# Kernel optimization log

Measured on AMD Instinct MI355X. Metric: run time of the kernel, lower is better.

Reference implementation:

```python
import jax, jax.numpy as jnp
import numpy as np

WINDOW_SIZE = 32  # band half-width = 16
EPS = 1e-5       # torch InstanceNorm1d default eps


def instance_norm_t(y):
    # y: (B, T, H); torch InstanceNorm1d (affine=False) normalizes each channel
    # over the temporal axis per sample, biased variance.
    m = jnp.mean(y, axis=1, keepdims=True)
    v = jnp.var(y, axis=1, keepdims=True)
    return (y - m) * jax.lax.rsqrt(v + EPS)


def setup_inputs() -> dict:
    key = jax.random.key(0)
    ks = jax.random.split(key, 7)
    B, T, IN, H = 4, 2048, 256, 256
    x = jax.random.normal(ks[0], (B, T, IN), dtype=jnp.float32)
    s = 0.02
    Wq = jax.random.normal(ks[1], (H, IN), dtype=jnp.float32) * s
    bq = jax.random.normal(ks[2], (H,), dtype=jnp.float32) * s
    Wk = jax.random.normal(ks[3], (H, IN), dtype=jnp.float32) * s
    bk = jax.random.normal(ks[4], (H,), dtype=jnp.float32) * s
    Wv = jax.random.normal(ks[5], (H, IN), dtype=jnp.float32) * s
    bv = jax.random.normal(ks[6], (H,), dtype=jnp.float32) * s
    return {"x": x, "Wq": Wq, "bq": bq, "Wk": Wk, "bk": bk, "Wv": Wv, "bv": bv}


def reference(x, Wq, bq, Wk, bk, Wv, bv):
    B, T, _ = x.shape
    H = Wq.shape[0]
    scale = H ** (-0.5)
    half = WINDOW_SIZE // 2  # 16

    q = instance_norm_t(x @ Wq.T + bq)  # (B, T, H)
    k = instance_norm_t(x @ Wk.T + bk)
    v = instance_norm_t(x @ Wv.T + bv)

    # Banded attention: for each query i only keys j with |i-j| <= half are live.
    offs = jnp.arange(-half, half + 1)                 # (W,) with W = 33
    idx = jnp.arange(T)[:, None] + offs[None, :]       # (T, W)
    valid = (idx >= 0) & (idx < T)                     # (T, W)
    idx_c = jnp.clip(idx, 0, T - 1)

    k_win = k[:, idx_c, :]                             # (B, T, W, H)
    v_win = v[:, idx_c, :]                             # (B, T, W, H)

    scores = jnp.einsum('bth,btwh->btw', q, k_win) * scale
    scores = jnp.where(valid[None], scores, -jnp.inf)
    probs = jax.nn.softmax(scores, axis=-1)            # (B, T, W)
    out = jnp.einsum('btw,btwh->bth', probs, v_win)    # (B, T, H)
    return jnp.mean(out, axis=1)                       # (B, H)
```

## Files before the change

kernel.cpp:

```cpp
#include <hip/hip_runtime.h>
#include <math.h>

#define BB 4
#define TT 2048
#define DIM 256
#define MROWS (BB*TT)
#define MN ((size_t)MROWS*DIM)
#define SCALE 0.0625f
#define HALF 16

typedef __attribute__((ext_vector_type(8))) short short8;
typedef __attribute__((ext_vector_type(4))) float f32x4;
typedef __attribute__((ext_vector_type(8))) unsigned short ushort8v;

__device__ __forceinline__ ushort f2bf(float f) {
    unsigned u = __builtin_bit_cast(unsigned, f);
    u += 0x7fffu + ((u >> 16) & 1u);
    return (ushort)(u >> 16);
}
__device__ __forceinline__ float bf2f(ushort u) {
    return __builtin_bit_cast(float, (unsigned)u << 16);
}
__device__ __forceinline__ unsigned cvtpk(float lo, float hi) {
    unsigned r;
    asm("v_cvt_pk_bf16_f32 %0, %1, %2" : "=v"(r) : "v"(lo), "v"(hi));
    return r;
}
__device__ __forceinline__ ushort8v pack8(f32x4 lo, f32x4 hi) {
    union { unsigned u[4]; ushort8v v; } r;
    r.u[0] = cvtpk(lo[0], lo[1]);
    r.u[1] = cvtpk(lo[2], lo[3]);
    r.u[2] = cvtpk(hi[0], hi[1]);
    r.u[3] = cvtpk(hi[2], hi[3]);
    return r.v;
}

#define GLOAD16(g, l) __builtin_amdgcn_global_load_lds( \
    (const __attribute__((address_space(1))) void*)(g), \
    (__attribute__((address_space(3))) void*)(l), 16, 0, 0)

#define LBAR() do { \
    asm volatile("s_waitcnt lgkmcnt(0)" ::: "memory"); \
    __builtin_amdgcn_s_barrier(); \
    __builtin_amdgcn_sched_barrier(0); \
} while (0)


#define A_TILE (128*64)
#define B_TILE (192*64)
__global__ __launch_bounds__(512) void gemm_kernel(
    const float* __restrict__ x,
    const float* __restrict__ Wq, const float* __restrict__ Wk, const float* __restrict__ Wv,
    const float* __restrict__ bq, const float* __restrict__ bk, const float* __restrict__ bv,
    ushort* __restrict__ qkv, float* __restrict__ part, float* __restrict__ out)
{
    __shared__ ushort As[2 * A_TILE];
    __shared__ ushort Bs[2 * B_TILE];
    __shared__ float sred[2][2][192];

    int tid = threadIdx.x;
    int lane = tid & 63, w = tid >> 6;
    int wr = w >> 2, wc = w & 3;

    int orig = blockIdx.x;
    if (orig == 0) {
        out[tid] = 0.f; out[512 + tid] = 0.f;
    }

    int wg = (orig & 7) * 32 + (orig >> 3);
    int mb = wg >> 2, nt = wg & 3;
    int m0 = mb * 128, n0 = nt * 192;

    int srow = lane >> 3;
    int sc   = lane & 7;
    int kof  = (sc ^ srow) << 3;
    const float* aRow = x + (size_t)(m0 + w * 16 + srow) * DIM + kof;
    const float* bRowP[3];
    #pragma unroll
    for (int g = 0; g < 3; g++) {
        int grow = n0 + w * 24 + g * 8 + srow;
        int whr = grow >> 8;
        const float* Wr = whr == 0 ? Wq : (whr == 1 ? Wk : Wv);
        bRowP[g] = Wr + (size_t)(grow & 255) * DIM + kof;
    }
    int aBase = (w * 16 + srow) * 64 + sc * 8;
    int bBase = (w * 24 + srow) * 64 + sc * 8;

    f32x4 acc[4][3] = {};
    f32x4 ra[2][2][2], rb[2][3][2];

    auto loadT = [&](int s, int kt) {
        int ko = kt * 64;
        #pragma unroll
        for (int g = 0; g < 2; g++) {
            ra[s][g][0] = *(const f32x4*)(aRow + (size_t)g * 8 * DIM + ko);
            ra[s][g][1] = *(const f32x4*)(aRow + (size_t)g * 8 * DIM + ko + 4);
        }
        #pragma unroll
        for (int g = 0; g < 3; g++) {
            rb[s][g][0] = *(const f32x4*)(bRowP[g] + ko);
            rb[s][g][1] = *(const f32x4*)(bRowP[g] + ko + 4);
        }
    };
    auto commitT = [&](int buf, int s) {
        ushort* Ab = &As[buf * A_TILE];
        ushort* Bb = &Bs[buf * B_TILE];
        #pragma unroll
        for (int g = 0; g < 2; g++)
            *(ushort8v*)(&Ab[aBase + g * 8 * 64]) = pack8(ra[s][g][0], ra[s][g][1]);
        #pragma unroll
        for (int g = 0; g < 3; g++)
            *(ushort8v*)(&Bb[bBase + g * 8 * 64]) = pack8(rb[s][g][0], rb[s][g][1]);
    };

    int fr = lane & 15, fp = lane >> 4, swz = lane & 7;

    loadT(0, 0);
    loadT(1, 1);
    commitT(0, 0);
    LBAR();
    #pragma unroll
    for (int kt = 0; kt < 4; kt++) {
        if (kt < 2) loadT(kt & 1, kt + 2);
        const ushort* a_lds = &As[(kt & 1) * A_TILE];
        const ushort* b_lds = &Bs[(kt & 1) * B_TILE];
        #pragma unroll
        for (int ks = 0; ks < 2; ks++) {
            short8 af[4], bf[3];
            #pragma unroll
            for (int i = 0; i < 4; i++) {
                int row = wr * 64 + i * 16 + fr;
                int slot = ks * 4 + fp;
                af[i] = *(const short8*)(&a_lds[row * 64 + ((slot ^ swz) << 3)]);
            }
            #pragma unroll
            for (int j = 0; j < 3; j++) {
                int row = wc * 48 + j * 16 + fr;
                int slot = ks * 4 + fp;
                bf[j] = *(const short8*)(&b_lds[row * 64 + ((slot ^ swz) << 3)]);
            }
            #pragma unroll
            for (int i = 0; i < 4; i++)
                #pragma unroll
                for (int j = 0; j < 3; j++)
                    acc[i][j] = __builtin_amdgcn_mfma_f32_16x16x32_bf16(
                        af[i], bf[j], acc[i][j], 0, 0, 0);
        }
        if (kt < 3) {
            commitT((kt + 1) & 1, (kt + 1) & 1);
            LBAR();
        }
    }
    __syncthreads();

    int b_idx = mb >> 4;
    int mb_local = mb & 15;
    #pragma unroll
    for (int j = 0; j < 3; j++) {
        int lstart = wc * 48 + j * 16;
        int gstart = n0 + lstart;
        int whf = gstart >> 8;
        int hbase = gstart & 255;
        const float* bias = whf == 0 ? bq : (whf == 1 ? bk : bv);
        int h = hbase + fr;
        float bb = bias[h];
        float s1 = 0.f, s2 = 0.f;
        ushort* outbase = qkv + (size_t)whf * MN + h;
        #pragma unroll
        for (int i = 0; i < 4; i++) {
            #pragma unroll
            for (int rr = 0; rr < 4; rr++) {
                int row = m0 + wr * 64 + i * 16 + fp * 4 + rr;
                float y = acc[i][j][rr] + bb;
                ushort ub = f2bf(y);
                outbase[(size_t)row * DIM] = ub;
                float yr = bf2f(ub);
                s1 += yr; s2 += yr * yr;
            }
        }
        s1 += __shfl_xor(s1, 16, 64); s1 += __shfl_xor(s1, 32, 64);
        s2 += __shfl_xor(s2, 16, 64); s2 += __shfl_xor(s2, 32, 64);
        if (fp == 0) { sred[0][wr][lstart + fr] = s1; sred[1][wr][lstart + fr] = s2; }
    }
    __syncthreads();
    if (tid < 192) {
        float p1 = sred[0][0][tid] + sred[0][1][tid];
        float p2 = sred[1][0][tid] + sred[1][1][tid];
        int gcol = n0 + tid;
        int whc = gcol >> 8, h = gcol & 255;
        int wb = whc * 4 + b_idx;
        part[((size_t)(wb * 2 + 0) * 256 + h) * 16 + mb_local] = p1;
        part[((size_t)(wb * 2 + 1) * 256 + h) * 16 + mb_local] = p2;
    }
}

__global__ __launch_bounds__(256) void attn_kernel(const ushort* __restrict__ qkv,
                                                   const float* __restrict__ part,
                                                   float* __restrict__ out)
{
    int orig = blockIdx.x + blockIdx.y * 64;
    int wg = (orig & 7) * 32 + (orig >> 3);
    int tile = wg & 63, b = wg >> 6;
    int t0 = tile * 32;

    const ushort* qg = qkv;
    const ushort* kg = qkv + MN;
    const ushort* vg = qkv + 2 * MN;

    __shared__ ushort Qs[32 * 256];
    __shared__ ushort Ks[64 * 256];
    __shared__ ushort Vs[64 * 256];
    __shared__ float Ps[32][65];
    __shared__ float csp[4][64];
    __shared__ float csum[64];
    __shared__ float qsc[256], qsh[256];

    int tid = threadIdx.x;
    int lane = tid & 63, w = tid >> 6;

    {
        int r0 = lane >> 5;
        int sp = lane & 31;
        #pragma unroll
        for (int i = 0; i < 8; i++) {
            int rowbase = (w * 8 + i) * 2;
            int r = rowbase + r0;
            int gt = t0 - HALF + r;
            int gtc = gt < 0 ? 0 : (gt > TT - 1 ? TT - 1 : gt);
            int s = sp ^ (r & 7);
            GLOAD16(kg + (size_t)(b * TT + gtc) * DIM + s * 8, &Ks[rowbase * 256]);
            GLOAD16(vg + (size_t)(b * TT + gtc) * DIM + sp * 8, &Vs[rowbase * 256]);
        }
    }

    float sums[3][2];
    #pragma unroll
    for (int wq = 0; wq < 3; wq++) {
        #pragma unroll
        for (int sm = 0; sm < 2; sm++) {
            const float* p = part + ((size_t)((wq * 4 + b) * 2 + sm) * 256 + tid) * 16;
            float a = 0.f;
            #pragma unroll
            for (int m4 = 0; m4 < 4; m4++) {
                f32x4 v = *(const f32x4*)(p + m4 * 4);
                a += (v[0] + v[1]) + (v[2] + v[3]);
            }
            sums[wq][sm] = a;
        }
    }
    float mq = sums[0][0] * (1.f / 2048.f);
    float rq = 1.f / sqrtf(sums[0][1] * (1.f / 2048.f) - mq * mq + 1e-5f);
    float mk = sums[1][0] * (1.f / 2048.f);
    float rk = 1.f / sqrtf(sums[1][1] * (1.f / 2048.f) - mk * mk + 1e-5f);
    float mv = sums[2][0] * (1.f / 2048.f);
    float rv = 1.f / sqrtf(sums[2][1] * (1.f / 2048.f) - mv * mv + 1e-5f);
    float qs = rq * rk;
    qsc[tid] = qs;  qsh[tid] = -mq * qs;
    float vscr = rv, vshr = -mv * rv;
    __syncthreads();

    #pragma unroll
    for (int i = 0; i < 4; i++) {
        int idx = tid + i * 256;
        int qr = idx >> 5, sp = idx & 31;
        int h0 = sp * 8;
        ushort8v raw = *(const ushort8v*)(qg + ((size_t)(b * TT + t0 + qr)) * DIM + h0);
        ushort8v o;
        #pragma unroll
        for (int e = 0; e < 8; e++)
            o[e] = f2bf(bf2f(raw[e]) * qsc[h0 + e] + qsh[h0 + e]);
        *(ushort8v*)(&Qs[qr * 256 + ((sp ^ (qr & 7)) << 3)]) = o;
    }
    __syncthreads();

    f32x4 sacc[2] = {};
    int fr = lane & 15, fp = lane >> 4, swz = lane & 7;
    int brow = w * 16 + fr;
    #pragma unroll
    for (int ks = 0; ks < 8; ks++) {
        int slot = ks * 4 + fp;
        short8 bfr = *(const short8*)(&Ks[brow * 256 + ((slot ^ swz) << 3)]);
        #pragma unroll
        for (int rf = 0; rf < 2; rf++) {
            int arow = rf * 16 + fr;
            short8 af = *(const short8*)(&Qs[arow * 256 + ((slot ^ swz) << 3)]);
            sacc[rf] = __builtin_amdgcn_mfma_f32_16x16x32_bf16(af, bfr, sacc[rf], 0, 0, 0);
        }
    }
    #pragma unroll
    for (int rf = 0; rf < 2; rf++)
        #pragma unroll
        for (int rr = 0; rr < 4; rr++)
            Ps[rf * 16 + fp * 4 + rr][w * 16 + fr] = sacc[rf][rr];
    __syncthreads();

    int r = tid >> 3, c0 = (tid & 7) * 8;
    float sv[8];
    float mx = -1e30f;
    #pragma unroll
    for (int j = 0; j < 8; j++) {
        int c = c0 + j;
        int gt = t0 - HALF + c;
        bool valid = (c >= r) && (c <= r + 32) && (gt >= 0) && (gt < TT);
        sv[j] = valid ? Ps[r][c] * SCALE : -1e30f;
        mx = fmaxf(mx, sv[j]);
    }
    #pragma unroll
    for (int d = 1; d < 8; d <<= 1) mx = fmaxf(mx, __shfl_xor(mx, d, 64));
    float sum = 0.f;
    #pragma unroll
    for (int j = 0; j < 8; j++) { sv[j] = __expf(sv[j] - mx); sum += sv[j]; }
    #pragma unroll
    for (int d = 1; d < 8; d <<= 1) sum += __shfl_xor(sum, d, 64);
    float inv = 1.0f / sum;
    #pragma unroll
    for (int j = 0; j < 8; j++) Ps[r][c0 + j] = sv[j] * inv;
    __syncthreads();

    {
        int c = tid & 63, rq4 = tid >> 6;
        float s = 0.f;
        #pragma unroll
        for (int j = 0; j < 8; j++) s += Ps[rq4 * 8 + j][c];
        csp[rq4][c] = s;
    }
    __syncthreads();
    if (tid < 64) csum[tid] = csp[0][tid] + csp[1][tid] + csp[2][tid] + csp[3][tid];
    __syncthreads();

    int h = tid;
    float o = 0.f;
    #pragma unroll 8
    for (int c = 0; c < 64; c++)
        o += csum[c] * bf2f(Vs[c * 256 + h]);
    o = vscr * o + 32.f * vshr;
    atomicAdd(&out[(size_t)b * DIM + h], o * (1.0f / TT));
}

extern "C" void kernel_launch(void* const* d_in, const int* in_sizes, int n_in,
                              void* d_out, int out_size, void* d_ws, size_t ws_size,
                              hipStream_t stream) {
    const float* x  = (const float*)d_in[0];
    const float* Wq = (const float*)d_in[1];
    const float* bq = (const float*)d_in[2];
    const float* Wk = (const float*)d_in[3];
    const float* bk = (const float*)d_in[4];
    const float* Wv = (const float*)d_in[5];
    const float* bv = (const float*)d_in[6];
    float* out = (float*)d_out;

    ushort* qkv  = (ushort*)d_ws;
    float* part  = (float*)(qkv + 3 * MN);

    gemm_kernel<<<dim3(256), 512, 0, stream>>>(x, Wq, Wk, Wv, bq, bk, bv, qkv, part, out);
    attn_kernel<<<dim3(64, 4), 256, 0, stream>>>(qkv, part, out);
}
```

Baseline: 23.27 us.

## Double attention kernel block size to 512 threads and redistribute work

```diff
diff --git a/kernel.cpp b/kernel.cpp
--- a/kernel.cpp
+++ b/kernel.cpp
@@ -194,7 +194,7 @@
     }
 }
 
-__global__ __launch_bounds__(256) void attn_kernel(const ushort* __restrict__ qkv,
+__global__ __launch_bounds__(512) void attn_kernel(const ushort* __restrict__ qkv,
                                                    const float* __restrict__ part,
                                                    float* __restrict__ out)
 {
@@ -211,9 +211,11 @@
     __shared__ ushort Ks[64 * 256];
     __shared__ ushort Vs[64 * 256];
     __shared__ float Ps[32][65];
-    __shared__ float csp[4][64];
+    __shared__ float csp[8][64];
     __shared__ float csum[64];
-    __shared__ float qsc[256], qsh[256];
+    __shared__ float sums_lds[6][256];
+    __shared__ float qsc[256], qsh[256], vsc[256], vsh[256];
+    __shared__ float osum[2][256];
 
     int tid = threadIdx.x;
     int lane = tid & 63, w = tid >> 6;
@@ -222,8 +224,8 @@
         int r0 = lane >> 5;
         int sp = lane & 31;
         #pragma unroll
-        for (int i = 0; i < 8; i++) {
-            int rowbase = (w * 8 + i) * 2;
+        for (int i = 0; i < 4; i++) {
+            int rowbase = (w * 4 + i) * 2;
             int r = rowbase + r0;
             int gt = t0 - HALF + r;
             int gtc = gt < 0 ? 0 : (gt > TT - 1 ? TT - 1 : gt);
@@ -233,35 +235,39 @@
         }
     }
 
-    float sums[3][2];
-    #pragma unroll
-    for (int wq = 0; wq < 3; wq++) {
-        #pragma unroll
-        for (int sm = 0; sm < 2; sm++) {
-            const float* p = part + ((size_t)((wq * 4 + b) * 2 + sm) * 256 + tid) * 16;
-            float a = 0.f;
-            #pragma unroll
-            for (int m4 = 0; m4 < 4; m4++) {
-                f32x4 v = *(const f32x4*)(p + m4 * 4);
-                a += (v[0] + v[1]) + (v[2] + v[3]);
-            }
-            sums[wq][sm] = a;
-        }
-    }
-    float mq = sums[0][0] * (1.f / 2048.f);
-    float rq = 1.f / sqrtf(sums[0][1] * (1.f / 2048.f) - mq * mq + 1e-5f);
-    float mk = sums[1][0] * (1.f / 2048.f);
-    float rk = 1.f / sqrtf(sums[1][1] * (1.f / 2048.f) - mk * mk + 1e-5f);
-    float mv = sums[2][0] * (1.f / 2048.f);
-    float rv = 1.f / sqrtf(sums[2][1] * (1.f / 2048.f) - mv * mv + 1e-5f);
-    float qs = rq * rk;
-    qsc[tid] = qs;  qsh[tid] = -mq * qs;
-    float vscr = rv, vshr = -mv * rv;
-    __syncthreads();
-
-    #pragma unroll
-    for (int i = 0; i < 4; i++) {
-        int idx = tid + i * 256;
+    #pragma unroll
+    for (int k = 0; k < 3; k++) {
+        int idx = tid + k * 512;
+        int ws_ = idx >> 8;
+        int h = idx & 255;
+        int wq = ws_ >> 1, sm = ws_ & 1;
+        const float* p = part + ((size_t)((wq * 4 + b) * 2 + sm) * 256 + h) * 16;
+        float a = 0.f;
+        #pragma unroll
+        for (int m4 = 0; m4 < 4; m4++) {
+            f32x4 v = *(const f32x4*)(p + m4 * 4);
+            a += (v[0] + v[1]) + (v[2] + v[3]);
+        }
+        sums_lds[ws_][h] = a;
+    }
+    __syncthreads();
+    if (tid < 256) {
+        int h = tid;
+        float mq = sums_lds[0][h] * (1.f / 2048.f);
+        float rq = 1.f / sqrtf(sums_lds[1][h] * (1.f / 2048.f) - mq * mq + 1e-5f);
+        float mk = sums_lds[2][h] * (1.f / 2048.f);
+        float rk = 1.f / sqrtf(sums_lds[3][h] * (1.f / 2048.f) - mk * mk + 1e-5f);
+        float mv = sums_lds[4][h] * (1.f / 2048.f);
+        float rv = 1.f / sqrtf(sums_lds[5][h] * (1.f / 2048.f) - mv * mv + 1e-5f);
+        float qs = rq * rk;
+        qsc[h] = qs;  qsh[h] = -mq * qs;
+        vsc[h] = rv;  vsh[h] = -mv * rv;
+    }
+    __syncthreads();
+
+    #pragma unroll
+    for (int i = 0; i < 2; i++) {
+        int idx = tid + i * 512;
         int qr = idx >> 5, sp = idx & 31;
         int h0 = sp * 8;
         ushort8v raw = *(const ushort8v*)(qg + ((size_t)(b * TT + t0 + qr)) * DIM + h0);
@@ -273,68 +279,77 @@
     }
     __syncthreads();
 
-    f32x4 sacc[2] = {};
-    int fr = lane & 15, fp = lane >> 4, swz = lane & 7;
-    int brow = w * 16 + fr;
-    #pragma unroll
-    for (int ks = 0; ks < 8; ks++) {
-        int slot = ks * 4 + fp;
-        short8 bfr = *(const short8*)(&Ks[brow * 256 + ((slot ^ swz) << 3)]);
-        #pragma unroll
-        for (int rf = 0; rf < 2; rf++) {
-            int arow = rf * 16 + fr;
-            short8 af = *(const short8*)(&Qs[arow * 256 + ((slot ^ swz) << 3)]);
-            sacc[rf] = __builtin_amdgcn_mfma_f32_16x16x32_bf16(af, bfr, sacc[rf], 0, 0, 0);
-        }
-    }
-    #pragma unroll
-    for (int rf = 0; rf < 2; rf++)
+    {
+        f32x4 sacc = {};
+        int fr = lane & 15, fp = lane >> 4, swz = lane & 7;
+        int brow = (w & 3) * 16 + fr;
+        int arow = (w >> 2) * 16 + fr;
+        #pragma unroll
+        for (int ks = 0; ks < 8; ks++) {
+            int slot = ks * 4 + fp;
+            short8 bfr = *(const short8*)(&Ks[brow * 256 + ((slot ^ swz) << 3)]);
+            short8 af  = *(const short8*)(&Qs[arow * 256 + ((slot ^ swz) << 3)]);
+            sacc = __builtin_amdgcn_mfma_f32_16x16x32_bf16(af, bfr, sacc, 0, 0, 0);
+        }
         #pragma unroll
         for (int rr = 0; rr < 4; rr++)
-            Ps[rf * 16 + fp * 4 + rr][w * 16 + fr] = sacc[rf][rr];
-    __syncthreads();
-
-    int r = tid >> 3, c0 = (tid & 7) * 8;
-    float sv[8];
-    float mx = -1e30f;
-    #pragma unroll
-    for (int j = 0; j < 8; j++) {
-        int c = c0 + j;
-        int gt = t0 - HALF + c;
-        bool valid = (c >= r) && (c <= r + 32) && (gt >= 0) && (gt < TT);
-        sv[j] = valid ? Ps[r][c] * SCALE : -1e30f;
-        mx = fmaxf(mx, sv[j]);
-    }
-    #pragma unroll
-    for (int d = 1; d < 8; d <<= 1) mx = fmaxf(mx, __shfl_xor(mx, d, 64));
-    float sum = 0.f;
-    #pragma unroll
-    for (int j = 0; j < 8; j++) { sv[j] = __expf(sv[j] - mx); sum += sv[j]; }
-    #pragma unroll
-    for (int d = 1; d < 8; d <<= 1) sum += __shfl_xor(sum, d, 64);
-    float inv = 1.0f / sum;
-    #pragma unroll
-    for (int j = 0; j < 8; j++) Ps[r][c0 + j] = sv[j] * inv;
-    __syncthreads();
-
-    {
-        int c = tid & 63, rq4 = tid >> 6;
+            Ps[(w >> 2) * 16 + fp * 4 + rr][(w & 3) * 16 + fr] = sacc[rr];
+    }
+    __syncthreads();
+
+    {
+        int r = tid >> 4, c0 = (tid & 15) * 4;
+        float sv[4];
+        float mx = -1e30f;
+        #pragma unroll
+        for (int j = 0; j < 4; j++) {
+            int c = c0 + j;
+            int gt = t0 - HALF + c;
+            bool valid = (c >= r) && (c <= r + 32) && (gt >= 0) && (gt < TT);
+            sv[j] = valid ? Ps[r][c] * SCALE : -1e30f;
+            mx = fmaxf(mx, sv[j]);
+        }
+        #pragma unroll
+        for (int d = 1; d < 16; d <<= 1) mx = fmaxf(mx, __shfl_xor(mx, d, 64));
+        float sum = 0.f;
+        #pragma unroll
+        for (int j = 0; j < 4; j++) { sv[j] = __expf(sv[j] - mx); sum += sv[j]; }
+        #pragma unroll
+        for (int d = 1; d < 16; d <<= 1) sum += __shfl_xor(sum, d, 64);
+        float inv = 1.0f / sum;
+        #pragma unroll
+        for (int j = 0; j < 4; j++) Ps[r][c0 + j] = sv[j] * inv;
+    }
+    __syncthreads();
+
+    {
+        int c = tid & 63, g = tid >> 6;
         float s = 0.f;
         #pragma unroll
-        for (int j = 0; j < 8; j++) s += Ps[rq4 * 8 + j][c];
-        csp[rq4][c] = s;
-    }
-    __syncthreads();
-    if (tid < 64) csum[tid] = csp[0][tid] + csp[1][tid] + csp[2][tid] + csp[3][tid];
-    __syncthreads();
-
-    int h = tid;
-    float o = 0.f;
-    #pragma unroll 8
-    for (int c = 0; c < 64; c++)
-        o += csum[c] * bf2f(Vs[c * 256 + h]);
-    o = vscr * o + 32.f * vshr;
-    atomicAdd(&out[(size_t)b * DIM + h], o * (1.0f / TT));
+        for (int j = 0; j < 4; j++) s += Ps[g * 4 + j][c];
+        csp[g][c] = s;
+    }
+    __syncthreads();
+    if (tid < 64)
+        csum[tid] = ((csp[0][tid] + csp[1][tid]) + (csp[2][tid] + csp[3][tid]))
+                  + ((csp[4][tid] + csp[5][tid]) + (csp[6][tid] + csp[7][tid]));
+    __syncthreads();
+
+    {
+        int h = tid & 255, half = tid >> 8;
+        float o = 0.f;
+        int cbase = half * 32;
+        #pragma unroll 8
+        for (int c = 0; c < 32; c++)
+            o += csum[cbase + c] * bf2f(Vs[(cbase + c) * 256 + h]);
+        osum[half][h] = o;
+    }
+    __syncthreads();
+    if (tid < 256) {
+        float oo = osum[0][tid] + osum[1][tid];
+        oo = vsc[tid] * oo + 32.f * vsh[tid];
+        atomicAdd(&out[(size_t)b * DIM + tid], oo * (1.0f / TT));
+    }
 }
 
 extern "C" void kernel_launch(void* const* d_in, const int* in_sizes, int n_in,
@@ -353,5 +368,5 @@
     float* part  = (float*)(qkv + 3 * MN);
 
     gemm_kernel<<<dim3(256), 512, 0, stream>>>(x, Wq, Wk, Wv, bq, bk, bv, qkv, part, out);
-    attn_kernel<<<dim3(64, 4), 256, 0, stream>>>(qkv, part, out);
-}
+    attn_kernel<<<dim3(64, 4), 512, 0, stream>>>(qkv, part, out);
+}
```

Result: faster. 22.50 us, median of 2 (-3.3%).
